# Kernel optimization log

Hardware: AMD Instinct MI355X
Metric: run time of the kernel (lower is better)

The kernel has to match this reference:

```python
import jax, jax.numpy as jnp
import numpy as np

IN_CH = 256
OUT_CH = 512
K = 4        # kernel_size (== input spatial size)
STRIDE = 1
PADDING = 0
GROUPS = 1
B = 32


def setup_inputs() -> dict:
    key = jax.random.key(0)
    ks = jax.random.split(key, 7)
    x = jax.random.normal(ks[0], (B, IN_CH, K, K), dtype=jnp.float32)
    s1 = 1.0 / np.sqrt(IN_CH)
    W1 = jax.random.normal(ks[1], (IN_CH, IN_CH), dtype=jnp.float32) * s1
    b1 = jax.random.normal(ks[2], (IN_CH,), dtype=jnp.float32) * s1
    W2 = jax.random.normal(ks[3], (OUT_CH * IN_CH, IN_CH), dtype=jnp.float32) * s1
    b2 = jax.random.normal(ks[4], (OUT_CH * IN_CH,), dtype=jnp.float32) * s1
    Wa = jax.random.normal(ks[5], (OUT_CH * IN_CH, IN_CH), dtype=jnp.float32) * s1
    ba = jax.random.normal(ks[6], (OUT_CH * IN_CH,), dtype=jnp.float32) * s1
    return {"x": x, "W1": W1, "b1": b1, "W2": W2, "b2": b2, "Wa": Wa, "ba": ba}


def _conv1x1(x, W, b):
    # x: [b, cin, h, w], W: [cout, cin], b: [cout]
    return jnp.einsum('bchw,oc->bohw', x, W) + b[None, :, None, None]


def reference(x, W1, b1, W2, b2, Wa, ba):
    b, c, h, w = x.shape  # h == w == K
    # AvgPool2d(K): non-overlapping K x K mean pooling -> [b, c, 1, 1] here
    avg = x.reshape(b, c, h // K, K, w // K, K).mean(axis=(3, 5))
    # attention branch (computed but unused downstream, as in original)
    att = jax.nn.sigmoid(_conv1x1(avg, Wa, ba))
    att = att.reshape(-1, IN_CH, K, K)
    # dynamic per-sample weights
    weight = jax.nn.relu(_conv1x1(x, W1, b1))
    weight = _conv1x1(weight, W2, b2)            # [b, OUT_CH*IN_CH, K, K]
    weight = weight.reshape(-1, IN_CH, K, K)     # [b*OUT_CH, IN_CH, K, K]
    # batch-as-groups grouped conv
    xg = x.reshape(1, b * c, h, w)
    out = jax.lax.conv_general_dilated(
        xg, weight,
        window_strides=(STRIDE, STRIDE),
        padding=[(PADDING, PADDING), (PADDING, PADDING)],
        dimension_numbers=('NCHW', 'OIHW', 'NCHW'),
        feature_group_count=GROUPS * b,
    )  # [1, b*OUT_CH, oh, ow]
    return out.reshape(b, OUT_CH, out.shape[-2], out.shape[-1])
```

## Files before the change

kernel.cpp:

```cpp
#include <hip/hip_runtime.h>

#define IC 256
#define OC 512
#define NB 32
#define NP 16
#define KTOT 65536
#define NKC 64
#define KCH 1024
#define KS2 64

__global__ void kA(const float* __restrict__ x, const float* __restrict__ W1,
                   const float* __restrict__ b1, float* __restrict__ h) {
    int bp = blockIdx.x;
    int b = bp >> 4, p = bp & 15;
    int c = threadIdx.x;
    __shared__ float xs[IC];
    xs[c] = x[b * 4096 + c * 16 + p];
    __syncthreads();
    float acc = b1[c];
    const float* wrow = W1 + c * IC;
    #pragma unroll 8
    for (int i = 0; i < IC; i += 4) {
        float4 w = *(const float4*)(wrow + i);
        acc += w.x * xs[i] + w.y * xs[i + 1] + w.z * xs[i + 2] + w.w * xs[i + 3];
    }
    h[b * 4096 + c * 16 + p] = fmaxf(acc, 0.f);
}

__global__ void kB(const float* __restrict__ x, const float* __restrict__ h,
                   float* __restrict__ Gt, float* __restrict__ sx) {
    int i = blockIdx.x;
    int c = threadIdx.x;
    __shared__ float xsh[NB * NP];
    for (int e = c; e < NB * NP; e += 256) {
        int b = e >> 4, p = e & 15;
        xsh[e] = x[b * 4096 + i * 16 + p];
    }
    __syncthreads();
    float g[NB];
    const float* hbase = h + c * 16;
    #pragma unroll 8
    for (int b = 0; b < NB; ++b) {
        float4 x0 = *(const float4*)&xsh[b * 16];
        float4 x1 = *(const float4*)&xsh[b * 16 + 4];
        float4 x2 = *(const float4*)&xsh[b * 16 + 8];
        float4 x3 = *(const float4*)&xsh[b * 16 + 12];
        const float* hp = hbase + b * 4096;
        float4 h0 = *(const float4*)(hp);
        float4 h1 = *(const float4*)(hp + 4);
        float4 h2 = *(const float4*)(hp + 8);
        float4 h3 = *(const float4*)(hp + 12);
        g[b] = x0.x * h0.x + x0.y * h0.y + x0.z * h0.z + x0.w * h0.w
             + x1.x * h1.x + x1.y * h1.y + x1.z * h1.z + x1.w * h1.w
             + x2.x * h2.x + x2.y * h2.y + x2.z * h2.z + x2.w * h2.w
             + x3.x * h3.x + x3.y * h3.y + x3.z * h3.z + x3.w * h3.w;
    }
    float* gout = Gt + (size_t)i * 8192 + (size_t)c * 32;
    #pragma unroll
    for (int j = 0; j < 8; ++j) {
        float4 v = make_float4(g[j * 4], g[j * 4 + 1], g[j * 4 + 2], g[j * 4 + 3]);
        *(float4*)(gout + j * 4) = v;
    }
    if (c < NB) {
        float s = 0.f;
        #pragma unroll
        for (int p = 0; p < 16; ++p) s += xsh[c * 16 + p];
        sx[c * IC + i] = s;
    }
}

__global__ void kC(const float* __restrict__ W2, const float* __restrict__ Gt,
                   float* __restrict__ partial) {
    __shared__ float w2s[KS2 * 65];
    __shared__ float gs[KS2 * 32];
    int tid = threadIdx.x;
    int kc = blockIdx.x;
    int o0 = blockIdx.y * 64;
    int k0 = kc * KCH;
    int bg = tid >> 5;
    int ov = tid & 31;
    int so = tid >> 4;
    int su = tid & 15;

    float acc[4][2];
    #pragma unroll
    for (int ii = 0; ii < 4; ++ii) { acc[ii][0] = 0.f; acc[ii][1] = 0.f; }

    for (int ks = 0; ks < KCH; ks += KS2) {
        __syncthreads();
        #pragma unroll
        for (int pass = 0; pass < 4; ++pass) {
            int o_l = so + pass * 16;
            float4 v = *(const float4*)(W2 + (size_t)(o0 + o_l) * KTOT + (k0 + ks + su * 4));
            float* dst = &w2s[o_l * 65 + su * 4];
            dst[0] = v.x; dst[1] = v.y; dst[2] = v.z; dst[3] = v.w;
        }
        #pragma unroll
        for (int pass = 0; pass < 2; ++pass) {
            int f = tid + pass * 256;
            *(float4*)&gs[f * 4] = *(const float4*)(Gt + (size_t)(k0 + ks) * 32 + f * 4);
        }
        __syncthreads();
        #pragma unroll 4
        for (int k = 0; k < KS2; ++k) {
            float4 g = *(float4*)&gs[k * 32 + bg * 4];
            float w0 = w2s[(ov * 2) * 65 + k];
            float w1 = w2s[(ov * 2 + 1) * 65 + k];
            acc[0][0] += g.x * w0; acc[0][1] += g.x * w1;
            acc[1][0] += g.y * w0; acc[1][1] += g.y * w1;
            acc[2][0] += g.z * w0; acc[2][1] += g.z * w1;
            acc[3][0] += g.w * w0; acc[3][1] += g.w * w1;
        }
    }
    float* pout = partial + (size_t)kc * 16384 + o0 + ov * 2;
    #pragma unroll
    for (int ii = 0; ii < 4; ++ii) {
        int b = bg * 4 + ii;
        *(float2*)(pout + b * 512) = make_float2(acc[ii][0], acc[ii][1]);
    }
}

__global__ void kBias(const float* __restrict__ b2, const float* __restrict__ sx,
                      float* __restrict__ bias) {
    __shared__ float sxs[32 * 260];
    __shared__ float b2s[8 * 260];
    int tid = threadIdx.x;
    int o0 = blockIdx.x * 8;
    #pragma unroll
    for (int p = 0; p < 32; ++p) {
        int f = tid + p * 256;
        sxs[(f >> 8) * 260 + (f & 255)] = sx[f];
    }
    #pragma unroll
    for (int p = 0; p < 8; ++p) {
        int f = tid + p * 256;
        b2s[(f >> 8) * 260 + (f & 255)] = b2[(size_t)o0 * 256 + f];
    }
    __syncthreads();
    int b = tid >> 3, ol = tid & 7;
    float acc = 0.f;
    #pragma unroll 8
    for (int i = 0; i < 256; i += 4) {
        float4 sv = *(float4*)&sxs[b * 260 + i];
        float4 wv = *(float4*)&b2s[ol * 260 + i];
        acc += sv.x * wv.x + sv.y * wv.y + sv.z * wv.z + sv.w * wv.w;
    }
    bias[b * 512 + o0 + ol] = acc;
}

__global__ void kRed(const float* __restrict__ partial, const float* __restrict__ bias,
                     float* __restrict__ out) {
    __shared__ float red[256];
    int tid = threadIdx.x;
    int q = tid >> 6, jj = tid & 63;
    int j = blockIdx.x * 64 + jj;
    float s = 0.f;
    #pragma unroll
    for (int t = 0; t < 16; ++t)
        s += partial[(size_t)(q * 16 + t) * 16384 + j];
    red[tid] = s;
    __syncthreads();
    if (tid < 64)
        out[j] = red[jj] + red[64 + jj] + red[128 + jj] + red[192 + jj] + bias[j];
}

extern "C" void kernel_launch(void* const* d_in, const int* in_sizes, int n_in,
                              void* d_out, int out_size, void* d_ws, size_t ws_size,
                              hipStream_t stream) {
    const float* x  = (const float*)d_in[0];
    const float* W1 = (const float*)d_in[1];
    const float* b1 = (const float*)d_in[2];
    const float* W2 = (const float*)d_in[3];
    const float* b2 = (const float*)d_in[4];
    float* out = (float*)d_out;
    float* ws = (float*)d_ws;

    float* h       = ws;
    float* sx      = ws + 131072;
    float* Gt      = ws + 139264;
    float* partial = ws + 2236416;
    float* bias    = ws;

    kA<<<NB * NP, 256, 0, stream>>>(x, W1, b1, h);
    kB<<<IC, 256, 0, stream>>>(x, h, Gt, sx);
    kBias<<<64, 256, 0, stream>>>(b2, sx, bias);
    kC<<<dim3(NKC, 8), 256, 0, stream>>>(W2, Gt, partial);
    kRed<<<256, 256, 0, stream>>>(partial, bias, out);
}
```

Baseline: 316.8 us.

## Restructure W2 GEMV kernel with register-blocked 4x32 tiles and direct weight streaming

The main kernel now streams W2 rows straight from global memory into registers, with software double-buffering of float4 loads, instead of staging them through shared memory. Each thread accumulates 4 output rows x 32 batches in registers, and lanes are reduced with shuffles. The K split grows from 64 to 256 chunks, so the partial buffer is larger and the reduction kernel sums 256 partials per output. This aims to cut LDS traffic and barriers on the bandwidth-bound 128 MB weight read, at the cost of high register pressure (128 accumulators) and more partial-sum traffic.

```diff
diff --git a/kernel.cpp b/kernel.cpp
--- a/kernel.cpp
+++ b/kernel.cpp
@@ -5,9 +5,8 @@
 #define NB 32
 #define NP 16
 #define KTOT 65536
-#define NKC 64
-#define KCH 1024
-#define KS2 64
+#define KCH2 256
+#define NKC2 256
 
 __global__ void kA(const float* __restrict__ x, const float* __restrict__ W1,
                    const float* __restrict__ b1, float* __restrict__ h) {
@@ -69,55 +68,98 @@
     }
 }
 
-__global__ void kC(const float* __restrict__ W2, const float* __restrict__ Gt,
-                   float* __restrict__ partial) {
-    __shared__ float w2s[KS2 * 65];
-    __shared__ float gs[KS2 * 32];
-    int tid = threadIdx.x;
-    int kc = blockIdx.x;
-    int o0 = blockIdx.y * 64;
-    int k0 = kc * KCH;
-    int bg = tid >> 5;
-    int ov = tid & 31;
-    int so = tid >> 4;
-    int su = tid & 15;
-
-    float acc[4][2];
-    #pragma unroll
-    for (int ii = 0; ii < 4; ++ii) { acc[ii][0] = 0.f; acc[ii][1] = 0.f; }
-
-    for (int ks = 0; ks < KCH; ks += KS2) {
-        __syncthreads();
-        #pragma unroll
-        for (int pass = 0; pass < 4; ++pass) {
-            int o_l = so + pass * 16;
-            float4 v = *(const float4*)(W2 + (size_t)(o0 + o_l) * KTOT + (k0 + ks + su * 4));
-            float* dst = &w2s[o_l * 65 + su * 4];
-            dst[0] = v.x; dst[1] = v.y; dst[2] = v.z; dst[3] = v.w;
-        }
-        #pragma unroll
-        for (int pass = 0; pass < 2; ++pass) {
-            int f = tid + pass * 256;
-            *(float4*)&gs[f * 4] = *(const float4*)(Gt + (size_t)(k0 + ks) * 32 + f * 4);
-        }
-        __syncthreads();
-        #pragma unroll 4
-        for (int k = 0; k < KS2; ++k) {
-            float4 g = *(float4*)&gs[k * 32 + bg * 4];
-            float w0 = w2s[(ov * 2) * 65 + k];
-            float w1 = w2s[(ov * 2 + 1) * 65 + k];
-            acc[0][0] += g.x * w0; acc[0][1] += g.x * w1;
-            acc[1][0] += g.y * w0; acc[1][1] += g.y * w1;
-            acc[2][0] += g.z * w0; acc[2][1] += g.z * w1;
-            acc[3][0] += g.w * w0; acc[3][1] += g.w * w1;
-        }
-    }
-    float* pout = partial + (size_t)kc * 16384 + o0 + ov * 2;
-    #pragma unroll
-    for (int ii = 0; ii < 4; ++ii) {
-        int b = bg * 4 + ii;
-        *(float2*)(pout + b * 512) = make_float2(acc[ii][0], acc[ii][1]);
-    }
+__global__ __launch_bounds__(256, 2)
+void kC(const float* __restrict__ W2, const float* __restrict__ Gt,
+        float* __restrict__ partial) {
+    __shared__ __align__(16) float gsh[KCH2 * 36];
+    const int kc = blockIdx.x;
+    const int ob = blockIdx.y;
+    const int tid = threadIdx.x;
+    const int j = tid & 3;
+    const int r = tid >> 2;
+    const int j4 = j * 4;
+    const int k0 = kc * KCH2;
+
+    {
+        const float* gsrc = Gt + (size_t)k0 * 32;
+        #pragma unroll
+        for (int c = 0; c < 8; ++c) {
+            int f = tid + c * 256;
+            float4 v = *(const float4*)(gsrc + (size_t)f * 4);
+            *(float4*)&gsh[(f >> 3) * 36 + (f & 7) * 4] = v;
+        }
+    }
+    __syncthreads();
+
+    const size_t orow = (size_t)(ob * 256 + r);
+    const float* w0 = W2 + (orow      ) * KTOT + k0 + j4;
+    const float* w1 = W2 + (orow +  64) * KTOT + k0 + j4;
+    const float* w2r= W2 + (orow + 128) * KTOT + k0 + j4;
+    const float* w3 = W2 + (orow + 192) * KTOT + k0 + j4;
+
+    float acc[4][32];
+    #pragma unroll
+    for (int rr = 0; rr < 4; ++rr)
+        #pragma unroll
+        for (int b = 0; b < 32; ++b) acc[rr][b] = 0.f;
+
+    auto body = [&](const float4 (&wv)[4], int kkv) {
+        const int kb = (kkv + j4) * 36;
+        #pragma unroll
+        for (int t = 0; t < 4; ++t) {
+            float4 gv[8];
+            #pragma unroll
+            for (int bq = 0; bq < 8; ++bq)
+                gv[bq] = *(const float4*)&gsh[kb + t * 36 + bq * 4];
+            #pragma unroll
+            for (int rr = 0; rr < 4; ++rr) {
+                float wt = (t == 0) ? wv[rr].x : (t == 1) ? wv[rr].y
+                         : (t == 2) ? wv[rr].z : wv[rr].w;
+                #pragma unroll
+                for (int bq = 0; bq < 8; ++bq) {
+                    acc[rr][bq * 4 + 0] = fmaf(wt, gv[bq].x, acc[rr][bq * 4 + 0]);
+                    acc[rr][bq * 4 + 1] = fmaf(wt, gv[bq].y, acc[rr][bq * 4 + 1]);
+                    acc[rr][bq * 4 + 2] = fmaf(wt, gv[bq].z, acc[rr][bq * 4 + 2]);
+                    acc[rr][bq * 4 + 3] = fmaf(wt, gv[bq].w, acc[rr][bq * 4 + 3]);
+                }
+            }
+        }
+    };
+
+    float4 wa[4], wb[4];
+    wa[0] = *(const float4*)(w0);  wa[1] = *(const float4*)(w1);
+    wa[2] = *(const float4*)(w2r); wa[3] = *(const float4*)(w3);
+
+    for (int kk = 0; kk < KCH2; kk += 32) {
+        wb[0] = *(const float4*)(w0 + kk + 16);
+        wb[1] = *(const float4*)(w1 + kk + 16);
+        wb[2] = *(const float4*)(w2r + kk + 16);
+        wb[3] = *(const float4*)(w3 + kk + 16);
+        body(wa, kk);
+        if (kk + 32 < KCH2) {
+            wa[0] = *(const float4*)(w0 + kk + 32);
+            wa[1] = *(const float4*)(w1 + kk + 32);
+            wa[2] = *(const float4*)(w2r + kk + 32);
+            wa[3] = *(const float4*)(w3 + kk + 32);
+        }
+        body(wb, kk + 16);
+    }
+
+    #pragma unroll
+    for (int rr = 0; rr < 4; ++rr)
+        #pragma unroll
+        for (int b = 0; b < 32; ++b) {
+            acc[rr][b] += __shfl_xor(acc[rr][b], 1, 64);
+            acc[rr][b] += __shfl_xor(acc[rr][b], 2, 64);
+        }
+
+    float* pout = partial + (size_t)kc * 16384 + ob * 256 + r;
+    #pragma unroll
+    for (int rr = 0; rr < 4; ++rr)
+        #pragma unroll
+        for (int b = 0; b < 32; ++b)
+            if ((b >> 3) == j)
+                pout[(size_t)b * 512 + rr * 64] = acc[rr][b];
 }
 
 __global__ void kBias(const float* __restrict__ b2, const float* __restrict__ sx,
@@ -155,9 +197,9 @@
     int q = tid >> 6, jj = tid & 63;
     int j = blockIdx.x * 64 + jj;
     float s = 0.f;
-    #pragma unroll
-    for (int t = 0; t < 16; ++t)
-        s += partial[(size_t)(q * 16 + t) * 16384 + j];
+    #pragma unroll 8
+    for (int t = 0; t < 64; ++t)
+        s += partial[(size_t)(q * 64 + t) * 16384 + j];
     red[tid] = s;
     __syncthreads();
     if (tid < 64)
@@ -184,6 +226,6 @@
     kA<<<NB * NP, 256, 0, stream>>>(x, W1, b1, h);
     kB<<<IC, 256, 0, stream>>>(x, h, Gt, sx);
     kBias<<<64, 256, 0, stream>>>(b2, sx, bias);
-    kC<<<dim3(NKC, 8), 256, 0, stream>>>(W2, Gt, partial);
+    kC<<<dim3(NKC2, 2), 256, 0, stream>>>(W2, Gt, partial);
     kRed<<<256, 256, 0, stream>>>(partial, bias, out);
 }
```

New measurement: 398.2 us. +25.7%, slower.
